# Optimization experiments

Measured on AMD Instinct MI355X. Metric: run time of the kernel, lower is better.

## Reference

```python
import jax, jax.numpy as jnp
import numpy as np

B, C_IN, HW, N = 128, 1024, 14, 196
D_MODEL, NH, HD, DFF = 384, 12, 32, 1536
ALPHA, BETA, GAMMA = 1.9, 3.8, 15.2
BETA_INT = int(BETA)          # 3
S = 2 * BETA_INT + 1          # 7
NUM_BUCKETS = S * S           # 49
BN_EPS = 2e-5


def _piecewise_index(d):
    # iRPE piecewise index (numpy, static): linear inside |d|<=alpha, log outside
    ad = np.abs(d).astype(np.float64)
    y = np.sign(d) * np.minimum(
        np.round(ALPHA + np.log(np.maximum(ad, ALPHA) / ALPHA) / np.log(GAMMA / ALPHA) * (BETA - ALPHA)),
        BETA)
    return np.where(ad <= ALPHA, d, y).astype(np.int64)  # trunc toward zero like torch .to(int)


def _make_rp_bucket():
    coords = np.stack(np.meshgrid(np.arange(HW), np.arange(HW), indexing='ij'), -1).reshape(-1, 2)
    diff = coords[:, None, :] - coords[None, :, :]  # [N,N,2]
    r = _piecewise_index(diff[..., 0]) + BETA_INT   # [0, 2*beta_int]
    c = _piecewise_index(diff[..., 1]) + BETA_INT
    return (r * S + c).astype(np.int32)            # [N,N] in [0,49)


RP_BUCKET = jnp.asarray(_make_rp_bucket())  # [196,196] int32, static


def _ln(x, w, b, eps=1e-5):
    mu = x.mean(-1, keepdims=True)
    var = ((x - mu) ** 2).mean(-1, keepdims=True)
    return (x - mu) * jax.lax.rsqrt(var + eps) * w + b


def setup_inputs() -> dict:
    key = jax.random.key(0)
    ks = jax.random.split(key, 12)
    g = lambda i, shape, s=0.02: jax.random.normal(ks[i], shape, jnp.float32) * s
    return {
        'x': jax.random.normal(ks[0], (B, C_IN, HW, HW), jnp.float32),
        'embed_fc1_w': g(1, (1024, C_IN)), 'embed_fc1_b': jnp.zeros((1024,), jnp.float32),
        'embed_fc2_w': g(2, (D_MODEL, 1024)), 'embed_fc2_b': jnp.zeros((D_MODEL,), jnp.float32),
        'pos_conv_w': g(3, (D_MODEL, 1, 3, 3), 0.1), 'pos_conv_b': jnp.zeros((D_MODEL,), jnp.float32),
        'ln1_w': jnp.ones((D_MODEL,), jnp.float32), 'ln1_b': jnp.zeros((D_MODEL,), jnp.float32),
        'qkv_w': g(4, (3 * D_MODEL, D_MODEL)),
        'rpe_table': g(5, (HD, NUM_BUCKETS)),
        'proj_w': g(6, (D_MODEL, D_MODEL)), 'proj_b': jnp.zeros((D_MODEL,), jnp.float32),
        'ln2_w': jnp.ones((D_MODEL,), jnp.float32), 'ln2_b': jnp.zeros((D_MODEL,), jnp.float32),
        'mlp_fc1_w': g(7, (DFF, D_MODEL)), 'mlp_fc1_b': jnp.zeros((DFF,), jnp.float32),
        'mlp_fc2_w': g(8, (D_MODEL, DFF)), 'mlp_fc2_b': jnp.zeros((D_MODEL,), jnp.float32),
        'bn1_w': jnp.ones((N,), jnp.float32), 'bn1_b': jnp.zeros((N,), jnp.float32),
        'lin_w': g(9, (D_MODEL, D_MODEL * N)), 'lin_b': jnp.zeros((D_MODEL,), jnp.float32),
        'bn2_w': jnp.ones((D_MODEL,), jnp.float32), 'bn2_b': jnp.zeros((D_MODEL,), jnp.float32),
    }


def reference(x, embed_fc1_w, embed_fc1_b, embed_fc2_w, embed_fc2_b,
              pos_conv_w, pos_conv_b, ln1_w, ln1_b, qkv_w, rpe_table,
              proj_w, proj_b, ln2_w, ln2_b, mlp_fc1_w, mlp_fc1_b,
              mlp_fc2_w, mlp_fc2_b, bn1_w, bn1_b, lin_w, lin_b, bn2_w, bn2_b):
    b = x.shape[0]
    # --- EmbedMLP: [B,C,14,14] -> [B,196,C] -> relu6 MLP -> [B,196,384]
    t = x.reshape(b, C_IN, N).transpose(0, 2, 1)
    t = jnp.clip(t @ embed_fc1_w.T + embed_fc1_b, 0.0, 6.0)
    t = t @ embed_fc2_w.T + embed_fc2_b
    # --- PosCNN: depthwise 3x3 conv + residual
    img = t.transpose(0, 2, 1).reshape(b, D_MODEL, HW, HW)
    conv = jax.lax.conv_general_dilated(
        img, pos_conv_w, (1, 1), 'SAME',
        dimension_numbers=('NCHW', 'OIHW', 'NCHW'), feature_group_count=D_MODEL)
    img = conv + pos_conv_b[None, :, None, None] + img
    t = img.reshape(b, D_MODEL, N).transpose(0, 2, 1)  # [B,196,384]
    # --- Attention with iRPE-on-k bias
    h = _ln(t, ln1_w, ln1_b)
    qkv = (h @ qkv_w.T).reshape(b, N, 3, NH, HD).transpose(2, 0, 3, 1, 4)
    scale = HD ** -0.5
    q = qkv[0] * scale
    k = qkv[1]
    v = qkv[2]
    attn = jnp.einsum('bhid,bhjd->bhij', q, k)
    # ctx-mode shared-head rpe_k: bias[b,h,i,j] = sum_d q[b,h,i,d] * table[d, bucket[i,j]]
    rpe_scores = jnp.einsum('bhid,dn->bhin', q, rpe_table)        # [B,H,N,49]
    bias = rpe_scores[:, :, jnp.arange(N)[:, None], RP_BUCKET]     # [B,H,N,N]
    attn = jax.nn.softmax(attn + bias, axis=-1)
    out = jnp.einsum('bhij,bhjd->bhid', attn, v)
    out = out.transpose(0, 2, 1, 3).reshape(b, N, D_MODEL)
    t = t + (out @ proj_w.T + proj_b)
    # --- MLP block
    h = _ln(t, ln2_w, ln2_b)
    h = jnp.clip(h @ mlp_fc1_w.T + mlp_fc1_b, 0.0, 6.0)
    t = t + (h @ mlp_fc2_w.T + mlp_fc2_b)
    # --- BatchNorm1d(196) over dims (batch, feature) per token channel (train-mode stats)
    mu = t.mean(axis=(0, 2), keepdims=True)
    var = t.var(axis=(0, 2), keepdims=True)
    t = (t - mu) * jax.lax.rsqrt(var + BN_EPS) * bn1_w[None, :, None] + bn1_b[None, :, None]
    # --- Flatten + Linear(196*384 -> 384)
    y = t.reshape(b, N * D_MODEL) @ lin_w.T + lin_b
    # --- BatchNorm1d(384) over batch (train-mode stats)
    mu2 = y.mean(axis=0, keepdims=True)
    var2 = y.var(axis=0, keepdims=True)
    y = (y - mu2) * jax.lax.rsqrt(var2 + BN_EPS) * bn2_w + bn2_b
    return y
```

## Files before the change

### kernel.cpp

```cpp
#include <hip/hip_runtime.h>
#include <cstdint>

#define B_    128
#define CIN   1024
#define NPOS  196
#define DM    384
#define NH_   12
#define HD_   32
#define DFF_  1536
#define MT    25088
#define SCALE_Q 0.17677669529663687f
#define SCALE2  0.25503485810335155f

typedef unsigned short u16;
typedef __attribute__((ext_vector_type(8))) short  short8;
typedef __attribute__((ext_vector_type(4))) float  f32x4;

__device__ __forceinline__ u16 f2bf(float f) {
  union { float f; uint32_t u; } v; v.f = f;
  uint32_t u = v.u;
  return (u16)((u + 0x7fffu + ((u >> 16) & 1u)) >> 16);
}
__device__ __forceinline__ float bf2f(u16 h) {
  union { uint32_t u; float f; } v; v.u = ((uint32_t)h) << 16;
  return v.f;
}

#define GLDS16(g, l)                                                           \
  __builtin_amdgcn_global_load_lds(                                            \
      (const __attribute__((address_space(1))) void*)(g),                      \
      (__attribute__((address_space(3))) void*)(l), 16, 0, 0)

template <int MODE>
__global__ __launch_bounds__(256) void gemm_k(
    const u16* __restrict__ A, const void* __restrict__ Wv,
    const float* __restrict__ bias, const float* __restrict__ res,
    void* __restrict__ outp,
    int M, int N, int K, int lda, int ldw, int nTN, int splitK)
{
  __shared__ __align__(16) u16 As[3][128 * 32];
  __shared__ __align__(16) u16 Bs[3][128 * 32];

  int nwg = gridDim.x;
  int bid0 = blockIdx.x;
  int qq = nwg >> 3, rr = nwg & 7;
  int xcd = bid0 & 7, idx = bid0 >> 3;
  int bid = (xcd < rr ? xcd * (qq + 1) : rr * (qq + 1) + (xcd - rr) * qq) + idx;

  int split = 0, mT, nT;
  if (MODE == 4) { split = bid / nTN; nT = bid % nTN; mT = 0; }
  else           { mT = bid / nTN;    nT = bid % nTN; }

  const u16* Ab = A + (size_t)split * splitK;
  float* outF = (float*)outp + ((MODE == 4) ? (size_t)split * (size_t)M * N : (size_t)0);
  u16*   outU = (u16*)outp;

  int tid = threadIdx.x;
  int wv = tid >> 6, ln = tid & 63;
  int q = ln >> 4, c = ln & 15;
  int wr = wv >> 1, wc = wv & 1;
  int mBase = mT * 128, nBase = nT * 128;

  f32x4 acc[4][4];
#pragma unroll
  for (int i = 0; i < 4; i++)
#pragma unroll
    for (int j = 0; j < 4; j++) acc[i][j] = (f32x4){0.f, 0.f, 0.f, 0.f};

  const u16* Ag = Ab + (size_t)mBase * lda;
  const u16*  Wg16 = (const u16*)Wv + (size_t)split * splitK + (size_t)nBase * ldw;
  const float* Wg32 = (const float*)Wv + (size_t)split * splitK + (size_t)nBase * ldw;

  int sl = ln & 3, rsub = ln >> 2;
  int lk = sl ^ ((rsub >> 1) & 3);

  float4 rbf[2][2];

  auto STAGE = [&](int t, int buf) {
    int k0 = t * 32;
#pragma unroll
    for (int i = 0; i < 2; i++) {
      int rb = wv * 32 + i * 16;
      GLDS16(Ag + (size_t)(rb + rsub) * lda + k0 + lk * 8, &As[buf][rb * 32]);
      if constexpr (MODE != 4)
        GLDS16(Wg16 + (size_t)(rb + rsub) * ldw + k0 + lk * 8, &Bs[buf][rb * 32]);
    }
  };
  auto LOADW = [&](int t) {
    int k0 = t * 32;
#pragma unroll
    for (int i = 0; i < 2; i++) {
      const float* wp = Wg32 + (size_t)(wv * 32 + i * 16 + rsub) * ldw + k0 + sl * 8;
      rbf[i][0] = *(const float4*)wp;
      rbf[i][1] = *(const float4*)(wp + 4);
    }
  };
  auto WRITEW = [&](int buf) {
#pragma unroll
    for (int i = 0; i < 2; i++) {
      int rloc = wv * 32 + i * 16 + rsub;
      short8 pk;
      pk[0] = (short)f2bf(rbf[i][0].x); pk[1] = (short)f2bf(rbf[i][0].y);
      pk[2] = (short)f2bf(rbf[i][0].z); pk[3] = (short)f2bf(rbf[i][0].w);
      pk[4] = (short)f2bf(rbf[i][1].x); pk[5] = (short)f2bf(rbf[i][1].y);
      pk[6] = (short)f2bf(rbf[i][1].z); pk[7] = (short)f2bf(rbf[i][1].w);
      *(short8*)&Bs[buf][rloc * 32 + (sl ^ ((rsub >> 1) & 3)) * 8] = pk;
    }
  };

  int NT = K >> 5;
  int ksw = (c >> 1) & 3;

  if constexpr (MODE == 4) {
    STAGE(0, 0);
    LOADW(0);
    WRITEW(0);
    asm volatile("s_waitcnt vmcnt(0) lgkmcnt(0)" ::: "memory");
    __builtin_amdgcn_s_barrier();
    int cur = 0;
    for (int t = 0; t < NT; ++t) {
      short8 afr[4], bfr[4];
#pragma unroll
      for (int mt2 = 0; mt2 < 4; mt2++)
        afr[mt2] = *(const short8*)&As[cur][(wr * 64 + mt2 * 16 + c) * 32 + (q ^ ksw) * 8];
#pragma unroll
      for (int nt2 = 0; nt2 < 4; nt2++)
        bfr[nt2] = *(const short8*)&Bs[cur][(wc * 64 + nt2 * 16 + c) * 32 + (q ^ ksw) * 8];
      asm volatile("s_waitcnt lgkmcnt(0)" ::: "memory");
      __builtin_amdgcn_sched_barrier(0);
      __builtin_amdgcn_s_barrier();
      if (t + 1 < NT) { STAGE(t + 1, cur ^ 1); LOADW(t + 1); WRITEW(cur ^ 1); }
      __builtin_amdgcn_sched_barrier(0);
#pragma unroll
      for (int mt2 = 0; mt2 < 4; mt2++)
#pragma unroll
        for (int nt2 = 0; nt2 < 4; nt2++)
          acc[mt2][nt2] = __builtin_amdgcn_mfma_f32_16x16x32_bf16(
              afr[mt2], bfr[nt2], acc[mt2][nt2], 0, 0, 0);
      if (t + 1 < NT) {
        asm volatile("s_waitcnt vmcnt(0) lgkmcnt(0)" ::: "memory");
        __builtin_amdgcn_s_barrier();
        cur ^= 1;
      }
    }
  } else {
    STAGE(0, 0);
    if (NT > 1) {
      STAGE(1, 1);
      asm volatile("s_waitcnt vmcnt(4)" ::: "memory");
    } else {
      asm volatile("s_waitcnt vmcnt(0)" ::: "memory");
    }
    __builtin_amdgcn_s_barrier();

    int cb = 0, sb = 2;
    for (int t = 0; t < NT; ++t) {
      short8 afr[4], bfr[4];
#pragma unroll
      for (int mt2 = 0; mt2 < 4; mt2++)
        afr[mt2] = *(const short8*)&As[cb][(wr * 64 + mt2 * 16 + c) * 32 + (q ^ ksw) * 8];
#pragma unroll
      for (int nt2 = 0; nt2 < 4; nt2++)
        bfr[nt2] = *(const short8*)&Bs[cb][(wc * 64 + nt2 * 16 + c) * 32 + (q ^ ksw) * 8];
      if (t + 2 < NT) STAGE(t + 2, sb);
      __builtin_amdgcn_sched_barrier(0);
#pragma unroll
      for (int mt2 = 0; mt2 < 4; mt2++)
#pragma unroll
        for (int nt2 = 0; nt2 < 4; nt2++)
          acc[mt2][nt2] = __builtin_amdgcn_mfma_f32_16x16x32_bf16(
              afr[mt2], bfr[nt2], acc[mt2][nt2], 0, 0, 0);
      if (t + 1 < NT) {
        if (t + 2 < NT)
          asm volatile("s_waitcnt vmcnt(4)" ::: "memory");
        else
          asm volatile("s_waitcnt vmcnt(0)" ::: "memory");
        __builtin_amdgcn_s_barrier();
      }
      cb = (cb == 2) ? 0 : cb + 1;
      sb = (sb == 2) ? 0 : sb + 1;
    }
  }

#pragma unroll
  for (int mt2 = 0; mt2 < 4; mt2++) {
    int row0 = mBase + wr * 64 + mt2 * 16 + q * 4;
#pragma unroll
    for (int nt2 = 0; nt2 < 4; nt2++) {
      int col = nBase + wc * 64 + nt2 * 16 + c;
      float bv = (MODE == 0 || MODE == 1 || MODE == 3) ? bias[col] : 0.f;
      f32x4 v = acc[mt2][nt2];
#pragma unroll
      for (int e = 0; e < 4; e++) {
        int row = row0 + e;
        float x = v[e] + bv;
        if (MODE == 0) x = fminf(fmaxf(x, 0.f), 6.f);
        if (MODE == 3) x += res[(size_t)row * N + col];
        if (MODE == 0 || MODE == 2) outU[(size_t)row * N + col] = f2bf(x);
        else                        outF[(size_t)row * N + col] = x;
      }
    }
  }
}

__global__ __launch_bounds__(224) void blut_k(uint8_t* __restrict__ lut)
{
  int i = blockIdx.x;
  int j = threadIdx.x;
  uint8_t v = 49;
  if (j < 196) {
    int ri = i / 14, ci = i - ri * 14;
    int rj = j / 14, cj = j - rj * 14;
    int dr = ri - rj, dc = ci - cj;
    int adr = dr < 0 ? -dr : dr, adc = dc < 0 ? -dc : dc;
    int tr = adr <= 1 ? adr : (adr <= 3 ? 2 : 3);
    int tc = adc <= 1 ? adc : (adc <= 3 ? 2 : 3);
    int fr = dr < 0 ? -tr : tr, fc = dc < 0 ? -tc : tc;
    v = (uint8_t)(fr * 7 + fc + 24);
  }
  lut[i * 224 + j] = v;
}

__global__ __launch_bounds__(256) void attn_k(
    const u16* __restrict__ QKV, const float* __restrict__ tabG,
    const uint8_t* __restrict__ lutG, u16* __restrict__ AO)
{
  __shared__ __align__(16) u16 Vt[32 * 228];
  __shared__ __align__(16) u16 Pc4[4][2][512];
  __shared__ __align__(16) u16 Ts[49 * 32];
  __shared__ __align__(16) u16 Rw4[4][2][16 * 50];
  int bh = blockIdx.x; int b = bh / NH_, h = bh % NH_;
  int tid = threadIdx.x;
  int wv = tid >> 6, ln = tid & 63;
  int q = ln >> 4, c = ln & 15;
  size_t rowbase = (size_t)b * NPOS * 1152 + h * 32;
  const u16* Kg = QKV + rowbase + 384;

  for (int t = tid; t < 49 * 32; t += 256) {
    int tt = t >> 5, k = t & 31;
    Ts[t] = f2bf(tabG[k * 49 + tt]);
  }
  for (int t = tid; t < 784; t += 256) {
    int nn = t >> 2, d0 = (t & 3) * 8;
    short8 v = *(const short8*)(QKV + rowbase + 768 + (size_t)nn * 1152 + d0);
#pragma unroll
    for (int j = 0; j < 8; j++) Vt[(d0 + j) * 228 + nn] = (u16)v[j];
  }
  for (int t = tid; t < 32 * 32; t += 256) {
    int d = t >> 5, jj = 196 + (t & 31);
    Vt[d * 228 + jj] = 0;
  }
  __syncthreads();

  for (int it = 0; it < 2; ++it) {
    int mtA = wv + it * 8;
    bool vB = (mtA + 4) < 13;
    int mbx[2];
    mbx[0] = mtA * 16;
    mbx[1] = (vB ? (mtA + 4) : 12) * 16;

    short8 afrag[2];
    int i0x[2], lutOff[2][4];
#pragma unroll
    for (int x = 0; x < 2; x++) {
      int irow = mbx[x] + c; if (irow > 195) irow = 195;
      afrag[x] = *(const short8*)(QKV + rowbase + (size_t)irow * 1152 + q * 8);
      i0x[x] = mbx[x] + q * 4;
#pragma unroll
      for (int e = 0; e < 4; e++) {
        int i = i0x[x] + e; if (i > 195) i = 195;
        lutOff[x][e] = i * 224;
      }
    }
    int rwOff[4];
#pragma unroll
    for (int e = 0; e < 4; e++) rwOff[e] = (q * 4 + e) * 50;

#pragma unroll
    for (int nt = 0; nt < 4; nt++) {
      int t = nt * 16 + c;
      int tt = t < 49 ? t : 48;
      short8 tb = *(const short8*)&Ts[tt * 32 + q * 8];
#pragma unroll
      for (int x = 0; x < 2; x++) {
        f32x4 z = {0.f, 0.f, 0.f, 0.f};
        f32x4 rr = __builtin_amdgcn_mfma_f32_16x16x32_bf16(afrag[x], tb, z, 0, 0, 0);
        if (t < 49) {
#pragma unroll
          for (int e = 0; e < 4; e++)
            Rw4[wv][x][rwOff[e] + t] = f2bf(rr[e] * SCALE2);
        }
      }
    }
    if (c == 0) {
#pragma unroll
      for (int x = 0; x < 2; x++)
#pragma unroll
        for (int e = 0; e < 4; e++)
          Rw4[wv][x][rwOff[e] + 49] = 0xFF80;
    }

    float mr[2] = {-INFINITY, -INFINITY};
    float l4[2][4] = {{0.f,0.f,0.f,0.f},{0.f,0.f,0.f,0.f}};
    f32x4 oacc[2][2];
#pragma unroll
    for (int x = 0; x < 2; x++) {
      oacc[x][0] = (f32x4){0.f, 0.f, 0.f, 0.f};
      oacc[x][1] = (f32x4){0.f, 0.f, 0.f, 0.f};
    }

    for (int ck = 0; ck < 7; ck++) {
      short8 bfr[2];
#pragma unroll
      for (int t = 0; t < 2; t++) {
        int j = (ck * 2 + t) * 16 + c;
        int jc = j > 195 ? 195 : j;
        bfr[t] = *(const short8*)(Kg + (size_t)jc * 1152 + q * 8);
      }
      f32x4 s01[2][2];
#pragma unroll
      for (int x = 0; x < 2; x++) {
        f32x4 z = {0.f, 0.f, 0.f, 0.f};
        s01[x][0] = __builtin_amdgcn_mfma_f32_16x16x32_bf16(afrag[x], bfr[0], z, 0, 0, 0);
        s01[x][1] = __builtin_amdgcn_mfma_f32_16x16x32_bf16(afrag[x], bfr[1], z, 0, 0, 0);
      }
      uint8_t bk[2][2][4];
#pragma unroll
      for (int t = 0; t < 2; t++) {
        int jj = ck * 32 + t * 16 + c;
#pragma unroll
        for (int x = 0; x < 2; x++)
#pragma unroll
          for (int e = 0; e < 4; e++) bk[x][t][e] = lutG[lutOff[x][e] + jj];
      }
#pragma unroll
      for (int x = 0; x < 2; x++)
#pragma unroll
        for (int t = 0; t < 2; t++)
#pragma unroll
          for (int e = 0; e < 4; e++)
            s01[x][t][e] = s01[x][t][e] * SCALE2 + bf2f(Rw4[wv][x][rwOff[e] + bk[x][t][e]]);

#pragma unroll
      for (int x = 0; x < 2; x++) {
        float mc = s01[x][0][0];
#pragma unroll
        for (int t = 0; t < 2; t++)
#pragma unroll
          for (int e = 0; e < 4; e++) mc = fmaxf(mc, s01[x][t][e]);
#pragma unroll
        for (int o = 1; o < 16; o <<= 1) mc = fmaxf(mc, __shfl_xor(mc, o, 64));
        float mn = fmaxf(mr[x], mc);
        float sc = __builtin_amdgcn_exp2f(mr[x] - mn);
        mr[x] = mn;
#pragma unroll
        for (int t = 0; t < 2; t++)
#pragma unroll
          for (int e = 0; e < 4; e++) s01[x][t][e] = __builtin_amdgcn_exp2f(s01[x][t][e] - mn);
#pragma unroll
        for (int e = 0; e < 4; e++) {
          l4[x][e] = l4[x][e] * sc + s01[x][0][e] + s01[x][1][e];
          oacc[x][0][e] *= sc; oacc[x][1][e] *= sc;
        }
#pragma unroll
        for (int t = 0; t < 2; t++) {
          int sl2 = t * 2 + (c >> 3);
#pragma unroll
          for (int e = 0; e < 4; e++) {
            union { float f; uint32_t u; } pv; pv.f = s01[x][t][e];
            Pc4[wv][x][(sl2 * 16 + q * 4 + e) * 8 + (c & 7)] = (u16)(pv.u >> 16);
          }
        }
      }
#pragma unroll
      for (int n2 = 0; n2 < 2; n2++) {
        short8 vb = *(const short8*)&Vt[(n2 * 16 + c) * 228 + ck * 32 + q * 8];
#pragma unroll
        for (int x = 0; x < 2; x++) {
          short8 pa = *(const short8*)&Pc4[wv][x][(q * 16 + c) * 8];
          oacc[x][n2] = __builtin_amdgcn_mfma_f32_16x16x32_bf16(pa, vb, oacc[x][n2], 0, 0, 0);
        }
      }
    }

#pragma unroll
    for (int x = 0; x < 2; x++) {
      if (x == 1 && !vB) continue;
      float inv[4];
#pragma unroll
      for (int e = 0; e < 4; e++) {
        float s2 = l4[x][e];
#pragma unroll
        for (int o = 1; o < 16; o <<= 1) s2 += __shfl_xor(s2, o, 64);
        inv[e] = 1.f / s2;
      }
#pragma unroll
      for (int n2 = 0; n2 < 2; n2++) {
#pragma unroll
        for (int e = 0; e < 4; e++) {
          int i = i0x[x] + e;
          if (i < 196) {
            int d = n2 * 16 + c;
            AO[((size_t)b * NPOS + i) * DM + h * 32 + d] = f2bf(oacc[x][n2][e] * inv[e]);
          }
        }
      }
    }
  }
}

__global__ __launch_bounds__(256) void transpose_cast_k(
    const float* __restrict__ x, u16* __restrict__ At)
{
  __shared__ float t[32][33];
  int c0 = blockIdx.x * 32, n0 = blockIdx.y * 32, b = blockIdx.z;
  int tx = threadIdx.x, ty = threadIdx.y;
  const float* xb = x + (size_t)b * CIN * NPOS;
#pragma unroll
  for (int i = 0; i < 4; i++) {
    int cc = c0 + ty + i * 8, nn = n0 + tx;
    t[ty + i * 8][tx] = (nn < NPOS) ? xb[(size_t)cc * NPOS + nn] : 0.f;
  }
  __syncthreads();
  u16* Ab = At + (size_t)b * NPOS * CIN;
#pragma unroll
  for (int i = 0; i < 4; i++) {
    int nn = n0 + ty + i * 8, cc = c0 + tx;
    if (nn < NPOS) Ab[(size_t)nn * CIN + cc] = f2bf(t[tx][ty + i * 8]);
  }
}

__global__ __launch_bounds__(256) void conv_res_k(
    const float* __restrict__ T0, const float* __restrict__ pcw,
    const float* __restrict__ pcb, float* __restrict__ T1)
{
  int idx = blockIdx.x * 256 + threadIdx.x;
  if (idx >= B_ * NPOS * 96) return;
  int d4 = idx % 96; int rem = idx / 96;
  int n = rem % NPOS; int b = rem / NPOS;
  int hh = n / 14, ww = n % 14;
  int d0 = d4 * 4;
  float w9[4][9];
#pragma unroll
  for (int j = 0; j < 4; j++)
#pragma unroll
    for (int t = 0; t < 9; t++) w9[j][t] = pcw[(d0 + j) * 9 + t];
  const float* base = T0 + (size_t)b * NPOS * DM;
  float4 ctr = *(const float4*)(base + (size_t)n * DM + d0);
  float ax = ctr.x + pcb[d0], ay = ctr.y + pcb[d0 + 1];
  float az = ctr.z + pcb[d0 + 2], aw = ctr.w + pcb[d0 + 3];
#pragma unroll
  for (int kh = 0; kh < 3; kh++) {
    int h2 = hh + kh - 1;
    if (h2 < 0 || h2 >= 14) continue;
#pragma unroll
    for (int kw = 0; kw < 3; kw++) {
      int w2 = ww + kw - 1;
      if (w2 < 0 || w2 >= 14) continue;
      float4 v = *(const float4*)(base + (size_t)(h2 * 14 + w2) * DM + d0);
      int t = kh * 3 + kw;
      ax += v.x * w9[0][t]; ay += v.y * w9[1][t];
      az += v.z * w9[2][t]; aw += v.w * w9[3][t];
    }
  }
  float4 o = {ax, ay, az, aw};
  *(float4*)(T1 + (size_t)b * NPOS * DM + (size_t)n * DM + d0) = o;
}

__global__ __launch_bounds__(256) void ln_k(
    const float* __restrict__ in, const float* __restrict__ w,
    const float* __restrict__ bb, u16* __restrict__ out)
{
  int row = blockIdx.x * 4 + (threadIdx.x >> 6);
  int ln = threadIdx.x & 63;
  const float2* r = (const float2*)(in + (size_t)row * DM);
  float2 v[3]; float s = 0.f, sq = 0.f;
#pragma unroll
  for (int j = 0; j < 3; j++) {
    v[j] = r[ln + 64 * j];
    s += v[j].x + v[j].y; sq += v[j].x * v[j].x + v[j].y * v[j].y;
  }
#pragma unroll
  for (int o = 1; o < 64; o <<= 1) { s += __shfl_xor(s, o, 64); sq += __shfl_xor(sq, o, 64); }
  float mu = s * (1.f / 384.f);
  float var = sq * (1.f / 384.f) - mu * mu;
  float rs = rsqrtf(var + 1e-5f);
  uint32_t* orow = (uint32_t*)(out + (size_t)row * DM);
#pragma unroll
  for (int j = 0; j < 3; j++) {
    int d = (ln + 64 * j) * 2;
    float a = (v[j].x - mu) * rs * w[d] + bb[d];
    float bq = (v[j].y - mu) * rs * w[d + 1] + bb[d + 1];
    orow[ln + 64 * j] = (uint32_t)f2bf(a) | ((uint32_t)f2bf(bq) << 16);
  }
}

__global__ __launch_bounds__(256) void bn1_partial_k(
    const float* __restrict__ T3, float* __restrict__ part)
{
  int n = blockIdx.x >> 3, g = blockIdx.x & 7;
  int tid = threadIdx.x;
  float s = 0.f, sq = 0.f;
  for (int b2 = g * 16; b2 < g * 16 + 16; b2++) {
    const float* p = T3 + ((size_t)b2 * NPOS + n) * DM;
    for (int d = tid; d < DM; d += 256) { float v = p[d]; s += v; sq += v * v; }
  }
#pragma unroll
  for (int o = 1; o < 64; o <<= 1) { s += __shfl_xor(s, o, 64); sq += __shfl_xor(sq, o, 64); }
  __shared__ float ls[4], lq[4];
  int wv = tid >> 6, ln = tid & 63;
  if (ln == 0) { ls[wv] = s; lq[wv] = sq; }
  __syncthreads();
  if (tid == 0) {
    part[blockIdx.x * 2]     = ls[0] + ls[1] + ls[2] + ls[3];
    part[blockIdx.x * 2 + 1] = lq[0] + lq[1] + lq[2] + lq[3];
  }
}

__global__ __launch_bounds__(256) void bn1_finish_k(
    const float* __restrict__ part, const float* __restrict__ bw,
    const float* __restrict__ bbb, float* __restrict__ scaleArr,
    float* __restrict__ shiftArr)
{
  int n = threadIdx.x;
  if (n >= NPOS) return;
  float S = 0.f, Q = 0.f;
#pragma unroll
  for (int g = 0; g < 8; g++) { S += part[(n * 8 + g) * 2]; Q += part[(n * 8 + g) * 2 + 1]; }
  float mu = S / 49152.f;
  float var = Q / 49152.f - mu * mu;
  float rs = rsqrtf(var + 2e-5f);
  float sc = rs * bw[n];
  scaleArr[n] = sc;
  shiftArr[n] = bbb[n] - mu * sc;
}

__global__ __launch_bounds__(256) void bn1_apply_k(
    const float* __restrict__ T3, const float* __restrict__ scaleArr,
    const float* __restrict__ shiftArr, u16* __restrict__ outb)
{
  int idx = blockIdx.x * 256 + threadIdx.x;
  if (idx >= MT * DM / 4) return;
  int n = (idx / 96) % NPOS;
  float4 v = *(const float4*)(T3 + (size_t)idx * 4);
  float sc = scaleArr[n], sh = shiftArr[n];
  uint32_t p0 = (uint32_t)f2bf(v.x * sc + sh) | ((uint32_t)f2bf(v.y * sc + sh) << 16);
  uint32_t p1 = (uint32_t)f2bf(v.z * sc + sh) | ((uint32_t)f2bf(v.w * sc + sh) << 16);
  ((uint2*)outb)[idx] = make_uint2(p0, p1);
}

__global__ __launch_bounds__(256) void lin_reduce_k(
    const float* __restrict__ part, const float* __restrict__ lb,
    float* __restrict__ y)
{
  int idx = blockIdx.x * 256 + threadIdx.x;
  if (idx >= 128 * DM) return;
  int col = idx % DM;
  float s = lb[col];
#pragma unroll
  for (int sp = 0; sp < 49; sp++) s += part[(size_t)sp * (128 * DM) + idx];
  y[idx] = s;
}

__global__ __launch_bounds__(64) void bn2_k(
    float* __restrict__ y, const float* __restrict__ w,
    const float* __restrict__ bb)
{
  int col = blockIdx.x; int ln = threadIdx.x;
  float v0 = y[(size_t)ln * DM + col];
  float v1 = y[(size_t)(ln + 64) * DM + col];
  float s = v0 + v1, sq = v0 * v0 + v1 * v1;
#pragma unroll
  for (int o = 1; o < 64; o <<= 1) { s += __shfl_xor(s, o, 64); sq += __shfl_xor(sq, o, 64); }
  float mu = s / 128.f;
  float var = sq / 128.f - mu * mu;
  float rs = rsqrtf(var + 2e-5f);
  float sc = rs * w[col], sh = bb[col] - mu * sc;
  y[(size_t)ln * DM + col] = v0 * sc + sh;
  y[(size_t)(ln + 64) * DM + col] = v1 * sc + sh;
}

__global__ __launch_bounds__(256) void castall_k(
    const float* __restrict__ s0, u16* __restrict__ d0,
    const float* __restrict__ s1, u16* __restrict__ d1,
    const float* __restrict__ s2, u16* __restrict__ d2,
    const float* __restrict__ s3, u16* __restrict__ d3,
    const float* __restrict__ s4, u16* __restrict__ d4,
    const float* __restrict__ s5, u16* __restrict__ d5)
{
  const int b0 = 262144, b1 = b0 + 98304, b2 = b1 + 110592,
            b3 = b2 + 36864, b4 = b3 + 147456, b5 = b4 + 147456;
  int idx = blockIdx.x * 256 + threadIdx.x;
  int stride = gridDim.x * 256;
  for (; idx < b5; idx += stride) {
    const float* s; u16* d; int l;
    if      (idx < b0) { s = s0; d = d0; l = idx; }
    else if (idx < b1) { s = s1; d = d1; l = idx - b0; }
    else if (idx < b2) { s = s2; d = d2; l = idx - b1; }
    else if (idx < b3) { s = s3; d = d3; l = idx - b2; }
    else if (idx < b4) { s = s4; d = d4; l = idx - b3; }
    else               { s = s5; d = d5; l = idx - b4; }
    float4 v = *(const float4*)(s + (size_t)l * 4);
    uint32_t p0 = (uint32_t)f2bf(v.x) | ((uint32_t)f2bf(v.y) << 16);
    uint32_t p1 = (uint32_t)f2bf(v.z) | ((uint32_t)f2bf(v.w) << 16);
    ((uint2*)d)[l] = make_uint2(p0, p1);
  }
}

extern "C" void kernel_launch(void* const* d_in, const int* in_sizes, int n_in,
                              void* d_out, int out_size, void* d_ws, size_t ws_size,
                              hipStream_t stream)
{
  (void)in_sizes; (void)n_in; (void)out_size;
  const float* x    = (const float*)d_in[0];
  const float* fc1w = (const float*)d_in[1];
  const float* fc1b = (const float*)d_in[2];
  const float* fc2w = (const float*)d_in[3];
  const float* fc2b = (const float*)d_in[4];
  const float* pcw  = (const float*)d_in[5];
  const float* pcb  = (const float*)d_in[6];
  const float* ln1w = (const float*)d_in[7];
  const float* ln1b = (const float*)d_in[8];
  const float* qkvw = (const float*)d_in[9];
  const float* rpet = (const float*)d_in[10];
  const float* projw= (const float*)d_in[11];
  const float* projb= (const float*)d_in[12];
  const float* ln2w = (const float*)d_in[13];
  const float* ln2b = (const float*)d_in[14];
  const float* m1w  = (const float*)d_in[15];
  const float* m1b  = (const float*)d_in[16];
  const float* m2w  = (const float*)d_in[17];
  const float* m2b  = (const float*)d_in[18];
  const float* bn1w = (const float*)d_in[19];
  const float* bn1b = (const float*)d_in[20];
  const float* linw = (const float*)d_in[21];
  const float* linb = (const float*)d_in[22];
  const float* bn2w = (const float*)d_in[23];
  const float* bn2b = (const float*)d_in[24];
  float* y = (float*)d_out;

  const size_t RA = 0;
  const size_t RB = 77070336;
  const size_t RC = RB + 57802752;
  const size_t RD = RC + 19267584;
  const size_t RE = RD + 38535168;
  const size_t RF = RE + 38535168;
  const size_t RG = RF + 9633792;
  const size_t RS = RG + 6422528;
  const size_t NEED = RS + 2048 + 16384 + 45056;
  if (ws_size < NEED) return;

  char* ws = (char*)d_ws;
  u16*   At    = (u16*)(ws + RA);
  u16*   MLP1  = (u16*)(ws + RA);
  u16*   U     = (u16*)(ws + RB);
  u16*   QKV   = (u16*)(ws + RB);
  u16*   T3nb  = (u16*)(ws + RB);
  u16*   H     = (u16*)(ws + RC);
  u16*   AO    = (u16*)(ws + RC);
  u16*   H2    = (u16*)(ws + RC);
  float* T0    = (float*)(ws + RD);
  float* T2    = (float*)(ws + RD);
  float* T1    = (float*)(ws + RE);
  float* T3    = (float*)(ws + RE);
  float* PART  = (float*)(ws + RF);
  u16*   wb_fc1 = (u16*)(ws + RG);
  u16*   wb_fc2 = wb_fc1 + 1048576;
  u16*   wb_qkv = wb_fc2 + 393216;
  u16*   wb_proj= wb_qkv + 442368;
  u16*   wb_m1  = wb_proj + 147456;
  u16*   wb_m2  = wb_m1 + 589824;
  float* bnS   = (float*)(ws + RS);
  float* bnSh  = bnS + 196;
  float* bnP   = (float*)(ws + RS + 2048);
  uint8_t* blut = (uint8_t*)(ws + RS + 2048 + 16384);

  castall_k<<<1024, 256, 0, stream>>>(fc1w, wb_fc1, fc2w, wb_fc2, qkvw, wb_qkv,
                                      projw, wb_proj, m1w, wb_m1, m2w, wb_m2);
  blut_k<<<196, 224, 0, stream>>>(blut);

  transpose_cast_k<<<dim3(32, 7, 128), dim3(32, 8), 0, stream>>>(x, At);

  gemm_k<0><<<196 * 8, 256, 0, stream>>>(At, wb_fc1, fc1b, nullptr, U,
                                          MT, 1024, 1024, 1024, 1024, 8, 0);
  gemm_k<1><<<196 * 3, 256, 0, stream>>>(U, wb_fc2, fc2b, nullptr, T0,
                                          MT, 384, 1024, 1024, 1024, 3, 0);
  conv_res_k<<<(B_ * NPOS * 96 + 255) / 256, 256, 0, stream>>>(T0, pcw, pcb, T1);
  ln_k<<<MT / 4, 256, 0, stream>>>(T1, ln1w, ln1b, H);
  gemm_k<2><<<196 * 9, 256, 0, stream>>>(H, wb_qkv, nullptr, nullptr, QKV,
                                          MT, 1152, 384, 384, 384, 9, 0);
  attn_k<<<1536, 256, 0, stream>>>(QKV, rpet, blut, AO);
  gemm_k<3><<<196 * 3, 256, 0, stream>>>(AO, wb_proj, projb, T1, T2,
                                          MT, 384, 384, 384, 384, 3, 0);
  ln_k<<<MT / 4, 256, 0, stream>>>(T2, ln2w, ln2b, H2);
  gemm_k<0><<<196 * 12, 256, 0, stream>>>(H2, wb_m1, m1b, nullptr, MLP1,
                                           MT, 1536, 384, 384, 384, 12, 0);
  gemm_k<3><<<196 * 3, 256, 0, stream>>>(MLP1, wb_m2, m2b, T2, T3,
                                          MT, 384, 1536, 1536, 1536, 3, 0);
  bn1_partial_k<<<196 * 8, 256, 0, stream>>>(T3, bnP);
  bn1_finish_k<<<1, 256, 0, stream>>>(bnP, bn1w, bn1b, bnS, bnSh);
  bn1_apply_k<<<(MT * DM / 4 + 255) / 256, 256, 0, stream>>>(T3, bnS, bnSh, T3nb);
  gemm_k<4><<<3 * 49, 256, 0, stream>>>(T3nb, linw, nullptr, nullptr, PART,
                                         128, 384, 1536, 75264, 75264, 3, 1536);
  lin_reduce_k<<<192, 256, 0, stream>>>(PART, linb, y);
  bn2_k<<<384, 64, 0, stream>>>(y, bn2w, bn2b);
}
```

Baseline: 546.0 us.

## Add 256x256-tile 8-wave pipelined GEMM for embed fc1 and MLP fc1

Adds a new 512-thread GEMM kernel with 256x256 output tiles, K-step 64, double-buffered LDS with XOR swizzle, and a four-phase schedule. Each phase interleaves MFMA with staged global-to-LDS loads and raises wave priority around the MFMA blocks. The kernel replaces the 128x128 gemm_k<0> for the two ReLU6 fc1 GEMMs (embed fc1 and MLP fc1). The goal is more data reuse per tile and better overlap of loads with compute. In exchange it launches fewer workgroups (392 and 588), which may underfill the CUs, and it uses more registers per thread.

```diff
diff --git a/kernel.cpp b/kernel.cpp
--- a/kernel.cpp
+++ b/kernel.cpp
@@ -30,6 +30,173 @@
   __builtin_amdgcn_global_load_lds(                                            \
       (const __attribute__((address_space(1))) void*)(g),                      \
       (__attribute__((address_space(3))) void*)(l), 16, 0, 0)
+
+template<int M0>
+__device__ __forceinline__ void phase_mfma(f32x4 (&acc)[8][4],
+                                           short8 (&a_)[2][2],
+                                           short8 (&b_)[4][2]) {
+#pragma unroll
+  for (int m2 = 0; m2 < 2; m2++)
+#pragma unroll
+    for (int n = 0; n < 4; n++)
+#pragma unroll
+      for (int ks = 0; ks < 2; ks++)
+        acc[M0 + m2][n] = __builtin_amdgcn_mfma_f32_16x16x32_bf16(
+            a_[m2][ks], b_[n][ks], acc[M0 + m2][n], 0, 0, 0);
+}
+
+__global__ __launch_bounds__(512) void gemm256_k(
+    const u16* __restrict__ A, const u16* __restrict__ W,
+    const float* __restrict__ bias, u16* __restrict__ out,
+    int M, int N, int K, int lda, int ldw, int nTN)
+{
+  __shared__ __align__(16) u16 As[2][2][8192];
+  __shared__ __align__(16) u16 Bs[2][2][8192];
+
+  int nwg = gridDim.x, bid0 = blockIdx.x;
+  int qq = nwg >> 3, rr = nwg & 7;
+  int xcd = bid0 & 7, idx = bid0 >> 3;
+  int bid = (xcd < rr ? xcd * (qq + 1) : rr * (qq + 1) + (xcd - rr) * qq) + idx;
+
+  int mT = bid / nTN, nT = bid % nTN;
+  int mBase = mT * 256, nBase = nT * 256;
+
+  int tid = threadIdx.x;
+  int w = tid >> 6, ln = tid & 63;
+  int q = ln >> 4, cc = ln & 15;
+  int wr = w >> 2, wc = w & 3;
+
+  const u16* Ag = A + (size_t)mBase * lda;
+  const u16* Wg = W + (size_t)nBase * ldw;
+
+  int srow = ln >> 2;
+  int skg  = ln & 3;
+
+  f32x4 acc[8][4];
+#pragma unroll
+  for (int i = 0; i < 8; i++)
+#pragma unroll
+    for (int j = 0; j < 4; j++) acc[i][j] = (f32x4){0.f, 0.f, 0.f, 0.f};
+
+  int NT = K >> 6;
+
+  auto STAGE_A = [&](int t, int half) {
+#pragma unroll
+    for (int i = 0; i < 2; i++) {
+      int c8 = w * 2 + i;
+      int h2 = c8 >> 3;
+      int row = ((c8 & 7) << 4) + srow;
+      int kg = skg ^ (((row >> 3) & 1) << 1);
+      GLDS16(Ag + (size_t)(half * 128 + row) * lda + t * 64 + h2 * 32 + kg * 8,
+             &As[t & 1][half][c8 << 9]);
+    }
+  };
+  auto STAGE_B = [&](int t, int half) {
+#pragma unroll
+    for (int i = 0; i < 2; i++) {
+      int c8 = w * 2 + i;
+      int h2 = c8 >> 3;
+      int row = ((c8 & 7) << 4) + srow;
+      int kg = skg ^ (((row >> 3) & 1) << 1);
+      GLDS16(Wg + (size_t)(half * 128 + row) * ldw + t * 64 + h2 * 32 + kg * 8,
+             &Bs[t & 1][half][c8 << 9]);
+    }
+  };
+
+  STAGE_A(0, 0); STAGE_A(0, 1); STAGE_B(0, 0); STAGE_B(0, 1);
+  if (NT > 1) {
+    STAGE_A(1, 0); STAGE_A(1, 1); STAGE_B(1, 0); STAGE_B(1, 1);
+    asm volatile("s_waitcnt vmcnt(8)" ::: "memory");
+  } else {
+    asm volatile("s_waitcnt vmcnt(0)" ::: "memory");
+  }
+  __builtin_amdgcn_s_barrier();
+
+  for (int t = 0; t < NT; ++t) {
+    int d = t & 1;
+    short8 b_[4][2], a_[2][2];
+
+    auto LOAD_A = [&](int m0) {
+      int fr0 = m0 * 16 + cc;
+      int sw0 = ((fr0 >> 3) & 1) << 1;
+      a_[0][0] = *(const short8*)&As[d][wr][fr0 * 32 + ((q ^ sw0) << 3)];
+      a_[0][1] = *(const short8*)&As[d][wr][4096 + fr0 * 32 + ((q ^ sw0) << 3)];
+      int fr1 = fr0 + 16;
+      int sw1 = ((fr1 >> 3) & 1) << 1;
+      a_[1][0] = *(const short8*)&As[d][wr][fr1 * 32 + ((q ^ sw1) << 3)];
+      a_[1][1] = *(const short8*)&As[d][wr][4096 + fr1 * 32 + ((q ^ sw1) << 3)];
+    };
+
+#pragma unroll
+    for (int n = 0; n < 4; n++) {
+      int fcl = (wc & 1) * 64 + n * 16 + cc;
+      int sw = ((fcl >> 3) & 1) << 1;
+      b_[n][0] = *(const short8*)&Bs[d][wc >> 1][fcl * 32 + ((q ^ sw) << 3)];
+      b_[n][1] = *(const short8*)&Bs[d][wc >> 1][4096 + fcl * 32 + ((q ^ sw) << 3)];
+    }
+    LOAD_A(0);
+    if (t >= 1 && t + 1 < NT) STAGE_A(t + 1, 0);
+    __builtin_amdgcn_s_barrier();
+    asm volatile("s_waitcnt lgkmcnt(0)" ::: "memory");
+    __builtin_amdgcn_sched_barrier(0);
+    __builtin_amdgcn_s_setprio(1);
+    phase_mfma<0>(acc, a_, b_);
+    __builtin_amdgcn_s_setprio(0);
+    __builtin_amdgcn_s_barrier();
+
+    LOAD_A(2);
+    if (t >= 1 && t + 1 < NT) STAGE_A(t + 1, 1);
+    __builtin_amdgcn_s_barrier();
+    asm volatile("s_waitcnt lgkmcnt(0)" ::: "memory");
+    __builtin_amdgcn_sched_barrier(0);
+    __builtin_amdgcn_s_setprio(1);
+    phase_mfma<2>(acc, a_, b_);
+    __builtin_amdgcn_s_setprio(0);
+    __builtin_amdgcn_s_barrier();
+
+    LOAD_A(4);
+    if (t + 2 < NT) STAGE_B(t + 2, 0);
+    __builtin_amdgcn_s_barrier();
+    asm volatile("s_waitcnt lgkmcnt(0)" ::: "memory");
+    __builtin_amdgcn_sched_barrier(0);
+    __builtin_amdgcn_s_setprio(1);
+    phase_mfma<4>(acc, a_, b_);
+    __builtin_amdgcn_s_setprio(0);
+    __builtin_amdgcn_s_barrier();
+
+    LOAD_A(6);
+    if (t + 2 < NT) STAGE_B(t + 2, 1);
+    __builtin_amdgcn_s_barrier();
+    asm volatile("s_waitcnt lgkmcnt(0)" ::: "memory");
+    __builtin_amdgcn_sched_barrier(0);
+    __builtin_amdgcn_s_setprio(1);
+    phase_mfma<6>(acc, a_, b_);
+    __builtin_amdgcn_s_setprio(0);
+    if (t + 1 < NT) {
+      if (t + 2 < NT)
+        asm volatile("s_waitcnt vmcnt(4)" ::: "memory");
+      else
+        asm volatile("s_waitcnt vmcnt(0)" ::: "memory");
+    }
+    __builtin_amdgcn_s_barrier();
+  }
+
+#pragma unroll
+  for (int m = 0; m < 8; m++) {
+    int row0 = mBase + wr * 128 + m * 16 + q * 4;
+#pragma unroll
+    for (int n = 0; n < 4; n++) {
+      int col = nBase + wc * 64 + n * 16 + cc;
+      float bv = bias[col];
+      f32x4 v = acc[m][n];
+#pragma unroll
+      for (int e = 0; e < 4; e++) {
+        float x = fminf(fmaxf(v[e] + bv, 0.f), 6.f);
+        out[(size_t)(row0 + e) * N + col] = f2bf(x);
+      }
+    }
+  }
+}
 
 template <int MODE>
 __global__ __launch_bounds__(256) void gemm_k(
@@ -681,8 +848,8 @@
 
   transpose_cast_k<<<dim3(32, 7, 128), dim3(32, 8), 0, stream>>>(x, At);
 
-  gemm_k<0><<<196 * 8, 256, 0, stream>>>(At, wb_fc1, fc1b, nullptr, U,
-                                          MT, 1024, 1024, 1024, 1024, 8, 0);
+  gemm256_k<<<98 * 4, 512, 0, stream>>>(At, wb_fc1, fc1b, U,
+                                        MT, 1024, 1024, 1024, 1024, 4);
   gemm_k<1><<<196 * 3, 256, 0, stream>>>(U, wb_fc2, fc2b, nullptr, T0,
                                           MT, 384, 1024, 1024, 1024, 3, 0);
   conv_res_k<<<(B_ * NPOS * 96 + 255) / 256, 256, 0, stream>>>(T0, pcw, pcb, T1);
@@ -693,8 +860,8 @@
   gemm_k<3><<<196 * 3, 256, 0, stream>>>(AO, wb_proj, projb, T1, T2,
                                           MT, 384, 384, 384, 384, 3, 0);
   ln_k<<<MT / 4, 256, 0, stream>>>(T2, ln2w, ln2b, H2);
-  gemm_k<0><<<196 * 12, 256, 0, stream>>>(H2, wb_m1, m1b, nullptr, MLP1,
-                                           MT, 1536, 384, 384, 384, 12, 0);
+  gemm256_k<<<98 * 6, 512, 0, stream>>>(H2, wb_m1, m1b, MLP1,
+                                        MT, 1536, 384, 384, 384, 6);
   gemm_k<3><<<196 * 3, 256, 0, stream>>>(MLP1, wb_m2, m2b, T2, T3,
                                           MT, 384, 1536, 1536, 1536, 3, 0);
   bn1_partial_k<<<196 * 8, 256, 0, stream>>>(T3, bnP);
```

New measurement: 540.8 us (median of 2 runs). No clear change (-1.0%).

## Add 256x256-tile 512-thread GEMM kernel for embed fc1 and MLP fc1

Applied to the files above, without the earlier changes.

Adds a new GEMM kernel with 256x256 output tiles, 8 waves each computing a 128x64 sub-tile, double-buffered LDS staging via global_load_lds, and a fused bias plus ReLU6 epilogue that writes bf16. It replaces the 128x128 template GEMM for the two wide-N layers (embed fc1 and MLP fc1) to raise arithmetic intensity and cut redundant global/LDS traffic. In exchange it uses more registers per thread (32 accumulator fragments) and launches fewer blocks, which may lower occupancy and latency hiding. It also drops the triple buffering of the old kernel and waits on all outstanding loads each k-step.

```diff
diff --git a/kernel.cpp b/kernel.cpp
--- a/kernel.cpp
+++ b/kernel.cpp
@@ -30,6 +30,97 @@
   __builtin_amdgcn_global_load_lds(                                            \
       (const __attribute__((address_space(1))) void*)(g),                      \
       (__attribute__((address_space(3))) void*)(l), 16, 0, 0)
+
+__global__ __launch_bounds__(512) void gemm256_k(
+    const u16* __restrict__ A, const u16* __restrict__ W,
+    const float* __restrict__ bias, u16* __restrict__ out,
+    int M, int N, int K, int lda, int ldw, int nTN)
+{
+  __shared__ __align__(16) u16 As[2][8192];
+  __shared__ __align__(16) u16 Bs[2][8192];
+
+  int nwg = gridDim.x, bid0 = blockIdx.x;
+  int qq = nwg >> 3, rr = nwg & 7;
+  int xcd = bid0 & 7, idx = bid0 >> 3;
+  int bid = (xcd < rr ? xcd * (qq + 1) : rr * (qq + 1) + (xcd - rr) * qq) + idx;
+
+  int mT = bid / nTN, nT = bid % nTN;
+  int mBase = mT * 256, nBase = nT * 256;
+
+  int tid = threadIdx.x;
+  int w = tid >> 6, ln = tid & 63;
+  int q = ln >> 4, c = ln & 15;
+  int wr = w >> 2, wc = w & 3;
+
+  const u16* Ag = A + (size_t)mBase * lda;
+  const u16* Wg = W + (size_t)nBase * ldw;
+
+  int sl = ln & 3, rsub = ln >> 2;
+  int lk = sl ^ ((rsub >> 1) & 3);
+
+  f32x4 acc[8][4];
+#pragma unroll
+  for (int i = 0; i < 8; i++)
+#pragma unroll
+    for (int j = 0; j < 4; j++) acc[i][j] = (f32x4){0.f, 0.f, 0.f, 0.f};
+
+  int NT = K >> 5;
+  int ksw = (c >> 1) & 3;
+
+  auto STAGE = [&](int t, int buf) {
+    int k0 = t * 32;
+#pragma unroll
+    for (int i = 0; i < 2; i++) {
+      int rb = (w * 2 + i) * 16;
+      GLDS16(Ag + (size_t)(rb + rsub) * lda + k0 + lk * 8, &As[buf][rb * 32]);
+      GLDS16(Wg + (size_t)(rb + rsub) * ldw + k0 + lk * 8, &Bs[buf][rb * 32]);
+    }
+  };
+
+  STAGE(0, 0);
+  asm volatile("s_waitcnt vmcnt(0)" ::: "memory");
+  __builtin_amdgcn_s_barrier();
+
+  int cur = 0;
+  for (int t = 0; t < NT; ++t) {
+    short8 afr[8], bfr[4];
+#pragma unroll
+    for (int m = 0; m < 8; m++)
+      afr[m] = *(const short8*)&As[cur][(wr * 128 + m * 16 + c) * 32 + ((q ^ ksw) << 3)];
+#pragma unroll
+    for (int n = 0; n < 4; n++)
+      bfr[n] = *(const short8*)&Bs[cur][(wc * 64 + n * 16 + c) * 32 + ((q ^ ksw) << 3)];
+    if (t + 1 < NT) STAGE(t + 1, cur ^ 1);
+    __builtin_amdgcn_sched_barrier(0);
+#pragma unroll
+    for (int m = 0; m < 8; m++)
+#pragma unroll
+      for (int n = 0; n < 4; n++)
+        acc[m][n] = __builtin_amdgcn_mfma_f32_16x16x32_bf16(
+            afr[m], bfr[n], acc[m][n], 0, 0, 0);
+    if (t + 1 < NT) {
+      asm volatile("s_waitcnt vmcnt(0)" ::: "memory");
+      __builtin_amdgcn_s_barrier();
+      cur ^= 1;
+    }
+  }
+
+#pragma unroll
+  for (int m = 0; m < 8; m++) {
+    int row0 = mBase + wr * 128 + m * 16 + q * 4;
+#pragma unroll
+    for (int n = 0; n < 4; n++) {
+      int col = nBase + wc * 64 + n * 16 + c;
+      float bv = bias[col];
+      f32x4 v = acc[m][n];
+#pragma unroll
+      for (int e = 0; e < 4; e++) {
+        float x = fminf(fmaxf(v[e] + bv, 0.f), 6.f);
+        out[(size_t)(row0 + e) * N + col] = f2bf(x);
+      }
+    }
+  }
+}
 
 template <int MODE>
 __global__ __launch_bounds__(256) void gemm_k(
@@ -681,8 +772,8 @@
 
   transpose_cast_k<<<dim3(32, 7, 128), dim3(32, 8), 0, stream>>>(x, At);
 
-  gemm_k<0><<<196 * 8, 256, 0, stream>>>(At, wb_fc1, fc1b, nullptr, U,
-                                          MT, 1024, 1024, 1024, 1024, 8, 0);
+  gemm256_k<<<98 * 4, 512, 0, stream>>>(At, wb_fc1, fc1b, U,
+                                        MT, 1024, 1024, 1024, 1024, 4);
   gemm_k<1><<<196 * 3, 256, 0, stream>>>(U, wb_fc2, fc2b, nullptr, T0,
                                           MT, 384, 1024, 1024, 1024, 3, 0);
   conv_res_k<<<(B_ * NPOS * 96 + 255) / 256, 256, 0, stream>>>(T0, pcw, pcb, T1);
@@ -693,8 +784,8 @@
   gemm_k<3><<<196 * 3, 256, 0, stream>>>(AO, wb_proj, projb, T1, T2,
                                           MT, 384, 384, 384, 384, 3, 0);
   ln_k<<<MT / 4, 256, 0, stream>>>(T2, ln2w, ln2b, H2);
-  gemm_k<0><<<196 * 12, 256, 0, stream>>>(H2, wb_m1, m1b, nullptr, MLP1,
-                                           MT, 1536, 384, 384, 384, 12, 0);
+  gemm256_k<<<98 * 6, 512, 0, stream>>>(H2, wb_m1, m1b, MLP1,
+                                        MT, 1536, 384, 384, 384, 6);
   gemm_k<3><<<196 * 3, 256, 0, stream>>>(MLP1, wb_m2, m2b, T2, T3,
                                           MT, 384, 1536, 1536, 1536, 3, 0);
   bn1_partial_k<<<196 * 8, 256, 0, stream>>>(T3, bnP);
```

Result: no change. 540.2 us (-1.1%).
